# Performance work log

Hardware: AMD Instinct MI355X
Metric: run time of the kernel (lower is better)

## Reference

```python
import jax, jax.numpy as jnp
import numpy as np

T, B, E, H = 2048, 2, 1024, 16
Dh = E // H


def setup_inputs() -> dict:
    key = jax.random.key(0)
    ks = jax.random.split(key, 5)
    s = 0.02
    query = jax.random.normal(ks[0], (T, B, E), dtype=jnp.float32)
    Wq = jax.random.normal(ks[1], (E, E), dtype=jnp.float32) * s
    Wk = jax.random.normal(ks[2], (E, E), dtype=jnp.float32) * s
    Wv = jax.random.normal(ks[3], (E, E), dtype=jnp.float32) * s
    Wo = jax.random.normal(ks[4], (E, E), dtype=jnp.float32) * s
    bq = jnp.zeros((E,), jnp.float32)
    bk = jnp.zeros((E,), jnp.float32)
    bv = jnp.zeros((E,), jnp.float32)
    bo = jnp.zeros((E,), jnp.float32)
    # additive causal mask: 0 on/below diagonal, -inf above (standard fairseq usage)
    neg = jnp.finfo(jnp.float32).min
    attn_mask = jnp.where(jnp.triu(jnp.ones((T, T), jnp.bool_), k=1), neg, 0.0).astype(jnp.float32)
    return {"query": query, "Wq": Wq, "bq": bq, "Wk": Wk, "bk": bk,
            "Wv": Wv, "bv": bv, "Wo": Wo, "bo": bo, "attn_mask": attn_mask}


def reference(query, Wq, bq, Wk, bk, Wv, bv, Wo, bo, attn_mask):
    t, b, e = query.shape
    scale = Dh ** -0.5
    # self-attention projections (nn.Linear: x @ W.T + b)
    q = (query @ Wq.T + bq) * scale  # [T,B,E]
    k = query @ Wk.T + bk
    v = query @ Wv.T + bv
    # [T, B*H, Dh] -> [B*H, T, Dh]
    q = q.reshape(t, b * H, Dh).transpose(1, 0, 2)
    k = k.reshape(t, b * H, Dh).transpose(1, 0, 2)
    v = v.reshape(t, b * H, Dh).transpose(1, 0, 2)
    # explicit bmm -> softmax -> bmm (materializes [B*H, T, T])
    attn_weights = jnp.einsum('btd,bsd->bts', q, k) + attn_mask[None, :, :]
    attn_probs = jax.nn.softmax(attn_weights, axis=-1)
    attn = jnp.einsum('bts,bsd->btd', attn_probs, v)  # [B*H, T, Dh]
    attn = attn.transpose(1, 0, 2).reshape(t, b, e)  # [T,B,E]
    out = attn @ Wo.T + bo
    return out
```

## Files before the change

### kernel.cpp

```cpp
#include <hip/hip_runtime.h>


typedef __attribute__((ext_vector_type(8))) short   s16x8;
typedef __attribute__((ext_vector_type(4))) float   f32x4;
typedef __attribute__((ext_vector_type(2))) __fp16  f16x2;
typedef __attribute__((ext_vector_type(4))) __fp16  f16x4;

#define MFMA16(a, b, c) __builtin_amdgcn_mfma_f32_16x16x32_bf16((a), (b), (c), 0, 0, 0)
#define MFMApv(a, b, c) __builtin_amdgcn_mfma_f32_16x16x16f16((a), (b), (c), 0, 0, 0)

static __device__ __forceinline__ unsigned short f2bf(float f) {
    unsigned u = __float_as_uint(f);
    unsigned r = u + 0x7fffu + ((u >> 16) & 1u);
    return (unsigned short)(r >> 16);
}

static __device__ __forceinline__ void gl2lds16(const void* g, void* l) {
    __builtin_amdgcn_global_load_lds(
        (const __attribute__((address_space(1))) unsigned int*)g,
        (__attribute__((address_space(3))) unsigned int*)l, 16, 0, 0);
}

__global__ __launch_bounds__(256) void cvt_all(const float* __restrict__ query,
                                               const float* __restrict__ w0,
                                               const float* __restrict__ w1,
                                               const float* __restrict__ w2,
                                               const float* __restrict__ w3,
                                               unsigned short* __restrict__ Xb,
                                               unsigned short* __restrict__ Wcat) {
    const int bx = blockIdx.x;
    if (bx < 4096) {
        const int i = threadIdx.x;
        const float4 f = reinterpret_cast<const float4*>(query + (size_t)bx * 1024)[i];
        ushort4 u;
        u.x = f2bf(f.x); u.y = f2bf(f.y); u.z = f2bf(f.z); u.w = f2bf(f.w);
        const int mrow = (bx & 1) * 2048 + (bx >> 1);
        reinterpret_cast<ushort4*>(Xb + (size_t)mrow * 1024)[i] = u;
    } else {
        const int j   = bx - 4096;
        const int sel = j >> 10;
        const int i   = (j & 1023) * 256 + threadIdx.x;
        const float* src = (sel == 0) ? w0 : (sel == 1) ? w1 : (sel == 2) ? w2 : w3;
        const float4 f = reinterpret_cast<const float4*>(src)[i];
        ushort4 u;
        u.x = f2bf(f.x); u.y = f2bf(f.y); u.z = f2bf(f.z); u.w = f2bf(f.w);
        reinterpret_cast<ushort4*>(Wcat + (size_t)sel * 1048576)[i] = u;
    }
}

__global__ __launch_bounds__(512, 2) void gemm_qkv(const unsigned short* __restrict__ A,
                                                   const unsigned short* __restrict__ W,
                                                   const float* __restrict__ b0,
                                                   const float* __restrict__ b1,
                                                   const float* __restrict__ b2,
                                                   unsigned short* __restrict__ outQK,
                                                   __fp16* __restrict__ outV) {
    __shared__ __align__(16) unsigned short smem[65536];

    const int tid  = threadIdx.x;
    const int w    = tid >> 6;
    const int lane = tid & 63;
    const int quad = lane >> 4;
    const int c    = lane & 15;
    const int wm   = w >> 2;
    const int wn   = w & 3;

    const int id   = blockIdx.x;
    const int xcd  = id & 7;
    const int slot = id >> 3;
    const int m0 = (xcd * 2 + (slot & 1)) * 256;
    const int n0 = (slot >> 1) * 256;

    f32x4 acc[8][4];
    #pragma unroll
    for (int mi = 0; mi < 8; ++mi)
        #pragma unroll
        for (int ni = 0; ni < 4; ++ni) acc[mi][ni] = (f32x4){0.f, 0.f, 0.f, 0.f};

    const int srow = tid >> 3;
    const int g    = (tid & 7) ^ (srow & 7);
    const unsigned short* aG = A + (size_t)(m0 + srow) * 1024 + g * 8;
    const unsigned short* wG = W + (size_t)(n0 + srow) * 1024 + g * 8;
    const int loff = tid * 8;

#define STA(buf, u, k0) gl2lds16(aG + (k0) + (u) * 65536, &smem[(buf) * 32768 + (u) * 4096 + loff])
#define STB(buf, u, k0) gl2lds16(wG + (k0) + (u) * 65536, &smem[(buf) * 32768 + 16384 + (u) * 4096 + loff])

    STB(0, 0, 0); STB(0, 1, 0); STB(0, 2, 0); STB(0, 3, 0);
    STA(0, 0, 0); STA(0, 2, 0); STA(0, 1, 0); STA(0, 3, 0);
    asm volatile("s_waitcnt vmcnt(2)" ::: "memory");
    asm volatile("s_barrier" ::: "memory");

    const int cs  = c & 7;
    const int ch0 = (quad ^ cs) << 3;
    const int ch1 = ((4 + quad) ^ cs) << 3;

    s16x8 af[4][2], bl[2][2], bh[2][2];

    #pragma unroll 1
    for (int t = 0; t < 16; ++t) {
        const unsigned short* Al = &smem[(t & 1) * 32768];
        const unsigned short* Bl = Al + 16384;
        const int  nb   = (t & 1) ^ 1;
        const int  kn   = (t + 1) * 64;
        const bool more = (t < 15);

        #pragma unroll
        for (int mi = 0; mi < 4; ++mi) {
            const int row = (wm * 128 + mi * 16 + c) * 64;
            af[mi][0] = *reinterpret_cast<const s16x8*>(&Al[row + ch0]);
            af[mi][1] = *reinterpret_cast<const s16x8*>(&Al[row + ch1]);
        }
        #pragma unroll
        for (int ni = 0; ni < 2; ++ni) {
            const int row = (wn * 64 + ni * 16 + c) * 64;
            bl[ni][0] = *reinterpret_cast<const s16x8*>(&Bl[row + ch0]);
            bl[ni][1] = *reinterpret_cast<const s16x8*>(&Bl[row + ch1]);
        }
        if (more) { STB(nb, 0, kn); STB(nb, 1, kn); }
        asm volatile("s_barrier" ::: "memory");
        __builtin_amdgcn_s_setprio(1);
        #pragma unroll
        for (int mi = 0; mi < 4; ++mi)
            #pragma unroll
            for (int ni = 0; ni < 2; ++ni) {
                acc[mi][ni] = MFMA16(af[mi][0], bl[ni][0], acc[mi][ni]);
                acc[mi][ni] = MFMA16(af[mi][1], bl[ni][1], acc[mi][ni]);
            }
        __builtin_amdgcn_s_setprio(0);
        asm volatile("s_barrier" ::: "memory");

        #pragma unroll
        for (int ni = 0; ni < 2; ++ni) {
            const int row = (wn * 64 + (2 + ni) * 16 + c) * 64;
            bh[ni][0] = *reinterpret_cast<const s16x8*>(&Bl[row + ch0]);
            bh[ni][1] = *reinterpret_cast<const s16x8*>(&Bl[row + ch1]);
        }
        if (more) { STB(nb, 2, kn); STB(nb, 3, kn); }
        asm volatile("s_barrier" ::: "memory");
        __builtin_amdgcn_s_setprio(1);
        #pragma unroll
        for (int mi = 0; mi < 4; ++mi)
            #pragma unroll
            for (int ni = 0; ni < 2; ++ni) {
                acc[mi][2 + ni] = MFMA16(af[mi][0], bh[ni][0], acc[mi][2 + ni]);
                acc[mi][2 + ni] = MFMA16(af[mi][1], bh[ni][1], acc[mi][2 + ni]);
            }
        __builtin_amdgcn_s_setprio(0);
        if (more) asm volatile("s_waitcnt vmcnt(4)" ::: "memory");
        else      asm volatile("s_waitcnt vmcnt(0)" ::: "memory");
        asm volatile("s_barrier" ::: "memory");

        #pragma unroll
        for (int mi = 0; mi < 4; ++mi) {
            const int row = (wm * 128 + (4 + mi) * 16 + c) * 64;
            af[mi][0] = *reinterpret_cast<const s16x8*>(&Al[row + ch0]);
            af[mi][1] = *reinterpret_cast<const s16x8*>(&Al[row + ch1]);
        }
        if (more) { STA(nb, 0, kn); STA(nb, 2, kn); }
        asm volatile("s_barrier" ::: "memory");
        __builtin_amdgcn_s_setprio(1);
        #pragma unroll
        for (int mi = 0; mi < 4; ++mi)
            #pragma unroll
            for (int ni = 0; ni < 2; ++ni) {
                acc[4 + mi][ni] = MFMA16(af[mi][0], bl[ni][0], acc[4 + mi][ni]);
                acc[4 + mi][ni] = MFMA16(af[mi][1], bl[ni][1], acc[4 + mi][ni]);
            }
        __builtin_amdgcn_s_setprio(0);
        asm volatile("s_barrier" ::: "memory");

        if (more) { STA(nb, 1, kn); STA(nb, 3, kn); }
        asm volatile("s_barrier" ::: "memory");
        __builtin_amdgcn_s_setprio(1);
        #pragma unroll
        for (int mi = 0; mi < 4; ++mi)
            #pragma unroll
            for (int ni = 0; ni < 2; ++ni) {
                acc[4 + mi][2 + ni] = MFMA16(af[mi][0], bh[ni][0], acc[4 + mi][2 + ni]);
                acc[4 + mi][2 + ni] = MFMA16(af[mi][1], bh[ni][1], acc[4 + mi][2 + ni]);
            }
        __builtin_amdgcn_s_setprio(0);
        if (more) asm volatile("s_waitcnt vmcnt(2)" ::: "memory");
        asm volatile("s_barrier" ::: "memory");
    }
#undef STA
#undef STB

    if (n0 < 2048) {
        const float scale = (n0 < 1024) ? 0.18033688011112042f : 1.0f;
        const float* bias = (n0 < 1024) ? b0 : b1;
        #pragma unroll
        for (int ni = 0; ni < 4; ++ni) {
            const int n = n0 + wn * 64 + ni * 16 + c;
            const float bval = bias[n & 1023];
            #pragma unroll
            for (int mi = 0; mi < 8; ++mi)
                #pragma unroll
                for (int r = 0; r < 4; ++r) {
                    const int m = m0 + wm * 128 + mi * 16 + quad * 4 + r;
                    outQK[(size_t)m * 2048 + n] = f2bf((acc[mi][ni][r] + bval) * scale);
                }
        }
    } else {
        __fp16* lds16 = reinterpret_cast<__fp16*>(smem);
        #pragma unroll 1
        for (int tn = 0; tn < 2; ++tn) {
            __syncthreads();
            if ((wn >> 1) == tn) {
                #pragma unroll
                for (int ni = 0; ni < 4; ++ni) {
                    const int nLoc = (wn & 1) * 64 + ni * 16 + c;
                    const float bval = b2[(n0 - 2048) + tn * 128 + nLoc];
                    #pragma unroll
                    for (int mi = 0; mi < 8; ++mi) {
                        const int mLoc = mi * 16 + quad * 4;
                        const f16x2 lo = __builtin_amdgcn_cvt_pkrtz(acc[mi][ni][0] + bval,
                                                                    acc[mi][ni][1] + bval);
                        const f16x2 hi = __builtin_amdgcn_cvt_pkrtz(acc[mi][ni][2] + bval,
                                                                    acc[mi][ni][3] + bval);
                        uint2 st;
                        st.x = __builtin_bit_cast(unsigned int, lo);
                        st.y = __builtin_bit_cast(unsigned int, hi);
                        const int phys = wm * 16384 + nLoc * 128 +
                                         (((mLoc >> 3) ^ (nLoc & 15)) << 3) + (mLoc & 7);
                        *reinterpret_cast<uint2*>(&lds16[phys]) = st;
                    }
                }
            }
            __syncthreads();
            const int np   = tid >> 1;
            const int rg   = np >> 7;
            const int nLoc = np & 127;
            const int vcol = (n0 - 2048) + tn * 128 + nLoc;
            const int bb = m0 >> 11;
            const int tbase = (m0 & 2047) + rg * 128;
            __fp16* vdst = outV + ((size_t)((bb * 16 + (vcol >> 6)) * 64 + (vcol & 63))) * 2048 + tbase;
            #pragma unroll
            for (int j = 0; j < 8; ++j) {
                const int lc = (tid & 1) * 8 + j;
                *reinterpret_cast<uint4*>(vdst + lc * 8) =
                    *reinterpret_cast<const uint4*>(
                        &lds16[rg * 16384 + nLoc * 128 + ((lc ^ (nLoc & 15)) << 3)]);
            }
        }
    }
}

__global__ __launch_bounds__(256) void gemm_out(const unsigned short* __restrict__ A,
                                                const unsigned short* __restrict__ W,
                                                const float* __restrict__ bias,
                                                float* __restrict__ outF) {
    __shared__ __align__(16) unsigned short Al[2][64 * 64];
    __shared__ __align__(16) unsigned short Bl[2][128 * 64];

    const int tid  = threadIdx.x;
    const int w    = tid >> 6;
    const int lane = tid & 63;
    const int quad = lane >> 4;
    const int c    = lane & 15;

    const int id   = blockIdx.x;
    const int xcd  = id & 7;
    const int slot = id >> 3;
    const int m0 = (xcd * 8 + (slot & 7)) * 64;
    const int n0 = (slot >> 3) * 128;

    f32x4 acc[8];
    #pragma unroll
    for (int ni = 0; ni < 8; ++ni) acc[ni] = (f32x4){0.f, 0.f, 0.f, 0.f};

    const int srow = tid >> 3;
    const int g    = (tid & 7) ^ (srow & 7);
    const unsigned short* aG = A + (size_t)(m0 + srow) * 1024 + g * 8;
    const unsigned short* wG = W + (size_t)(n0 + srow) * 1024 + g * 8;
    const int loff = tid * 8;

    const int cs = (c & 7);

    gl2lds16(aG,             &Al[0][loff]);
    gl2lds16(aG + 32 * 1024, &Al[0][loff + 2048]);
    #pragma unroll
    for (int i = 0; i < 4; ++i)
        gl2lds16(wG + i * 32 * 1024, &Bl[0][loff + i * 2048]);

    #pragma unroll 1
    for (int kk = 0; kk < 16; ++kk) {
        __syncthreads();
        if (kk < 15) {
            const int k0n = (kk + 1) * 64;
            const int nb  = (kk + 1) & 1;
            gl2lds16(aG + k0n,             &Al[nb][loff]);
            gl2lds16(aG + k0n + 32 * 1024, &Al[nb][loff + 2048]);
            #pragma unroll
            for (int i = 0; i < 4; ++i)
                gl2lds16(wG + k0n + i * 32 * 1024, &Bl[nb][loff + i * 2048]);
        }
        const int cb = kk & 1;
        const int arow = (w * 16 + c) * 64;
        const s16x8 af0 = *reinterpret_cast<const s16x8*>(&Al[cb][arow + ((quad ^ cs) << 3)]);
        const s16x8 af1 = *reinterpret_cast<const s16x8*>(&Al[cb][arow + (((4 + quad) ^ cs) << 3)]);
        __builtin_amdgcn_s_setprio(1);
        #pragma unroll
        for (int ni = 0; ni < 8; ++ni) {
            const int brow = (ni * 16 + c) * 64;
            const s16x8 bf0 = *reinterpret_cast<const s16x8*>(&Bl[cb][brow + ((quad ^ cs) << 3)]);
            const s16x8 bf1 = *reinterpret_cast<const s16x8*>(&Bl[cb][brow + (((4 + quad) ^ cs) << 3)]);
            acc[ni] = MFMA16(af0, bf0, acc[ni]);
            acc[ni] = MFMA16(af1, bf1, acc[ni]);
        }
        __builtin_amdgcn_s_setprio(0);
    }

    #pragma unroll
    for (int ni = 0; ni < 8; ++ni) {
        const int n = n0 + ni * 16 + c;
        const float bval = bias[n];
        const int m = m0 + w * 16 + quad * 4;
        const int bb = m >> 11, t = m & 2047;
        #pragma unroll
        for (int r = 0; r < 4; ++r)
            outF[(size_t)(2 * (t + r) + bb) * 1024 + n] = acc[ni][r] + bval;
    }
}

__global__ __launch_bounds__(256, 4) void attn_kernel(const unsigned short* __restrict__ QKb,
                                                      const __fp16* __restrict__ Vt,
                                                      unsigned short* __restrict__ Ob) {
    __shared__ unsigned short Kl[2][2][64][32];
    __shared__ __fp16 Vl[2][64][64];

    const int tid  = threadIdx.x;
    const int w    = tid >> 6;
    const int lane = tid & 63;
    const int quad = lane >> 4;
    const int c    = lane & 15;

    const int id = blockIdx.x;
    const int bh = (id & 7) * 4 + ((id >> 3) & 3);
    const int kidx = id >> 5;
    const int rr   = kidx >> 3, jj = kidx & 7;
    const int a    = (rr & 1) ? (24 - 8 * rr + jj) : (31 - 8 * rr - jj);
    const int bB = bh >> 4, h = bh & 15;
    const int t0 = a * 64;
    const int trg = t0 + w * 16;
    const int nIt = a + 1;

    const unsigned short* qp = QKb + (size_t)(bB * 2048 + trg + c) * 2048 + h * 64 + quad * 8;
    const s16x8 aq0 = *reinterpret_cast<const s16x8*>(qp);
    const s16x8 aq1 = *reinterpret_cast<const s16x8*>(qp + 32);

    const int lr4 = lane >> 2, sl4 = lane & 3;
    const unsigned short* kSrc = QKb + (size_t)(bB * 2048 + w * 16 + lr4) * 2048
                                 + 1024 + h * 64 + (sl4 ^ ((lane >> 3) & 3)) * 8;
    const int vr8 = lane >> 3, sl8 = lane & 7;
    const __fp16* vSrcA = Vt + (size_t)(bh * 64 + w * 16 + vr8) * 2048 + (sl8 ^ vr8) * 8;
    const __fp16* vSrcB = vSrcA + (size_t)8 * 2048;

    f32x4 acc[4];
    float l = 0.f;
    #pragma unroll
    for (int dt = 0; dt < 4; ++dt) acc[dt] = (f32x4){0.f, 0.f, 0.f, 0.f};

    const int kswz = (quad ^ ((c >> 1) & 3)) * 8;

    {
        gl2lds16(kSrc,      &Kl[0][0][w * 16 + lr4][sl4 * 8]);
        gl2lds16(kSrc + 32, &Kl[0][1][w * 16 + lr4][sl4 * 8]);
        gl2lds16(vSrcA,     &Vl[0][w * 16 + vr8][sl8 * 8]);
        gl2lds16(vSrcB,     &Vl[0][w * 16 + 8 + vr8][sl8 * 8]);
    }

    for (int it = 0; it < nIt; ++it) {
        const int buf = it & 1;
        __syncthreads();
        if (it + 1 < nIt) {
            const size_t s1 = (size_t)(it + 1) * 64;
            const int nb = buf ^ 1;
            gl2lds16(kSrc + s1 * 2048,      &Kl[nb][0][w * 16 + lr4][sl4 * 8]);
            gl2lds16(kSrc + s1 * 2048 + 32, &Kl[nb][1][w * 16 + lr4][sl4 * 8]);
            gl2lds16(vSrcA + s1,            &Vl[nb][w * 16 + vr8][sl8 * 8]);
            gl2lds16(vSrcB + s1,            &Vl[nb][w * 16 + 8 + vr8][sl8 * 8]);
        }

        s16x8 kf[4][2];
        #pragma unroll
        for (int ns = 0; ns < 4; ++ns) {
            kf[ns][0] = *reinterpret_cast<const s16x8*>(&Kl[buf][0][ns * 16 + c][kswz]);
            kf[ns][1] = *reinterpret_cast<const s16x8*>(&Kl[buf][1][ns * 16 + c][kswz]);
        }
        f16x4 vf[4][4];
        #pragma unroll
        for (int dt = 0; dt < 4; ++dt)
            #pragma unroll
            for (int ch = 0; ch < 4; ++ch) {
                const int phys = ((2 * ch + (quad >> 1)) ^ (c & 7)) * 8 + (quad & 1) * 4;
                vf[dt][ch] = *reinterpret_cast<const f16x4*>(&Vl[buf][dt * 16 + c][phys]);
            }

        const int s0 = it * 64;
        const bool diag = (it == a);
        f32x4 sT[4];
        __builtin_amdgcn_s_setprio(1);
        #pragma unroll
        for (int ns = 0; ns < 4; ++ns) {
            f32x4 z = (f32x4){0.f, 0.f, 0.f, 0.f};
            z = MFMA16(kf[ns][0], aq0, z);
            sT[ns] = MFMA16(kf[ns][1], aq1, z);
        }
        __builtin_amdgcn_s_setprio(0);
        f16x4 pf[4];
        float lp = 0.f;
        #pragma unroll
        for (int ns = 0; ns < 4; ++ns) {
            float pv[4];
            #pragma unroll
            for (int r = 0; r < 4; ++r) pv[r] = __builtin_amdgcn_exp2f(sT[ns][r]);
            if (diag) {
                const int sb = s0 + ns * 16 + quad * 4;
                const int qg = trg + c;
                #pragma unroll
                for (int r = 0; r < 4; ++r) if (sb + r > qg) pv[r] = 0.f;
            }
            lp += (pv[0] + pv[1]) + (pv[2] + pv[3]);
            const f16x2 lo = __builtin_amdgcn_cvt_pkrtz(pv[0], pv[1]);
            const f16x2 hi = __builtin_amdgcn_cvt_pkrtz(pv[2], pv[3]);
            pf[ns] = __builtin_shufflevector(lo, hi, 0, 1, 2, 3);
        }
        l += lp;
        __builtin_amdgcn_s_setprio(1);
        #pragma unroll
        for (int dt = 0; dt < 4; ++dt)
            #pragma unroll
            for (int ns = 0; ns < 4; ++ns)
                acc[dt] = MFMApv(vf[dt][ns], pf[ns], acc[dt]);
        __builtin_amdgcn_s_setprio(0);
    }

    float lv = l;
    lv += __shfl_xor(lv, 16);
    lv += __shfl_xor(lv, 32);
    const float inv = 1.0f / lv;
    const size_t base = (size_t)(bB * 2048 + trg + c) * 1024 + h * 64;
    #pragma unroll
    for (int dt = 0; dt < 4; ++dt) {
        const unsigned u0 = (unsigned)f2bf(acc[dt][0] * inv)
                          | ((unsigned)f2bf(acc[dt][1] * inv) << 16);
        const unsigned u1 = (unsigned)f2bf(acc[dt][2] * inv)
                          | ((unsigned)f2bf(acc[dt][3] * inv) << 16);
        uint2 st; st.x = u0; st.y = u1;
        *reinterpret_cast<uint2*>(Ob + base + dt * 16 + quad * 4) = st;
    }
}

extern "C" void kernel_launch(void* const* d_in, const int* in_sizes, int n_in,
                              void* d_out, int out_size, void* d_ws, size_t ws_size,
                              hipStream_t stream) {
    const float* query = (const float*)d_in[0];
    const float* Wq    = (const float*)d_in[1];
    const float* bq    = (const float*)d_in[2];
    const float* Wk    = (const float*)d_in[3];
    const float* bk    = (const float*)d_in[4];
    const float* Wv    = (const float*)d_in[5];
    const float* bv    = (const float*)d_in[6];
    const float* Wo    = (const float*)d_in[7];
    const float* bo    = (const float*)d_in[8];

    float* out = (float*)d_out;

    unsigned short* ws    = (unsigned short*)d_ws;
    unsigned short* Xbf   = ws;
    unsigned short* Wcat  = Xbf  + (size_t)4096 * 1024;
    unsigned short* QKb   = Wcat + (size_t)4 * 1024 * 1024;
    __fp16*         Vtw   = (__fp16*)(QKb + (size_t)4096 * 2048);
    unsigned short* attnb = (unsigned short*)(Vtw + (size_t)32 * 64 * 2048);

    cvt_all<<<8192, 256, 0, stream>>>(query, Wq, Wk, Wv, Wo, Xbf, Wcat);

    gemm_qkv<<<192, 512, 0, stream>>>(Xbf, Wcat, bq, bk, bv, QKb, Vtw);

    attn_kernel<<<1024, 256, 0, stream>>>(QKb, Vtw, attnb);

    gemm_out<<<512, 256, 0, stream>>>(attnb, Wcat + (size_t)3 * 1024 * 1024,
                                      bo, out);
}
```

Before: 195.6 us.

## Restructure QKV GEMM main loop with full-tile prefetch and fewer barriers

New measurement: 193.5 us. No clear change (-1.1%).

```diff
diff --git a/kernel.cpp b/kernel.cpp
--- a/kernel.cpp
+++ b/kernel.cpp
@@ -95,94 +95,80 @@
     const int ch0 = (quad ^ cs) << 3;
     const int ch1 = ((4 + quad) ^ cs) << 3;
 
-    s16x8 af[4][2], bl[2][2], bh[2][2];
+    s16x8 af[4][2], bf[4][2];
+
+    #pragma unroll
+    for (int mi = 0; mi < 4; ++mi) {
+        const int row = (wm * 128 + mi * 16 + c) * 64;
+        af[mi][0] = *reinterpret_cast<const s16x8*>(&smem[row + ch0]);
+        af[mi][1] = *reinterpret_cast<const s16x8*>(&smem[row + ch1]);
+    }
+    #pragma unroll
+    for (int ni = 0; ni < 4; ++ni) {
+        const int row = (wn * 64 + ni * 16 + c) * 64;
+        bf[ni][0] = *reinterpret_cast<const s16x8*>(&smem[16384 + row + ch0]);
+        bf[ni][1] = *reinterpret_cast<const s16x8*>(&smem[16384 + row + ch1]);
+    }
 
     #pragma unroll 1
     for (int t = 0; t < 16; ++t) {
         const unsigned short* Al = &smem[(t & 1) * 32768];
-        const unsigned short* Bl = Al + 16384;
         const int  nb   = (t & 1) ^ 1;
         const int  kn   = (t + 1) * 64;
         const bool more = (t < 15);
 
+        if (more) {
+            STB(nb, 0, kn); STB(nb, 1, kn); STB(nb, 2, kn); STB(nb, 3, kn);
+            STA(nb, 0, kn); STA(nb, 2, kn); STA(nb, 1, kn); STA(nb, 3, kn);
+        }
+
+        __builtin_amdgcn_s_setprio(1);
+        #pragma unroll
+        for (int mi = 0; mi < 4; ++mi)
+            #pragma unroll
+            for (int ni = 0; ni < 4; ++ni) {
+                acc[mi][ni] = MFMA16(af[mi][0], bf[ni][0], acc[mi][ni]);
+                acc[mi][ni] = MFMA16(af[mi][1], bf[ni][1], acc[mi][ni]);
+            }
+        __builtin_amdgcn_s_setprio(0);
+
+        if (more) asm volatile("s_waitcnt vmcnt(8)" ::: "memory");
+        else      asm volatile("s_waitcnt vmcnt(0)" ::: "memory");
+        asm volatile("s_barrier" ::: "memory");
+
         #pragma unroll
         for (int mi = 0; mi < 4; ++mi) {
-            const int row = (wm * 128 + mi * 16 + c) * 64;
+            const int row = (wm * 128 + 64 + mi * 16 + c) * 64;
             af[mi][0] = *reinterpret_cast<const s16x8*>(&Al[row + ch0]);
             af[mi][1] = *reinterpret_cast<const s16x8*>(&Al[row + ch1]);
         }
-        #pragma unroll
-        for (int ni = 0; ni < 2; ++ni) {
-            const int row = (wn * 64 + ni * 16 + c) * 64;
-            bl[ni][0] = *reinterpret_cast<const s16x8*>(&Bl[row + ch0]);
-            bl[ni][1] = *reinterpret_cast<const s16x8*>(&Bl[row + ch1]);
-        }
-        if (more) { STB(nb, 0, kn); STB(nb, 1, kn); }
-        asm volatile("s_barrier" ::: "memory");
         __builtin_amdgcn_s_setprio(1);
         #pragma unroll
         for (int mi = 0; mi < 4; ++mi)
             #pragma unroll
-            for (int ni = 0; ni < 2; ++ni) {
-                acc[mi][ni] = MFMA16(af[mi][0], bl[ni][0], acc[mi][ni]);
-                acc[mi][ni] = MFMA16(af[mi][1], bl[ni][1], acc[mi][ni]);
+            for (int ni = 0; ni < 4; ++ni) {
+                acc[4 + mi][ni] = MFMA16(af[mi][0], bf[ni][0], acc[4 + mi][ni]);
+                acc[4 + mi][ni] = MFMA16(af[mi][1], bf[ni][1], acc[4 + mi][ni]);
             }
         __builtin_amdgcn_s_setprio(0);
-        asm volatile("s_barrier" ::: "memory");
-
-        #pragma unroll
-        for (int ni = 0; ni < 2; ++ni) {
-            const int row = (wn * 64 + (2 + ni) * 16 + c) * 64;
-            bh[ni][0] = *reinterpret_cast<const s16x8*>(&Bl[row + ch0]);
-            bh[ni][1] = *reinterpret_cast<const s16x8*>(&Bl[row + ch1]);
-        }
-        if (more) { STB(nb, 2, kn); STB(nb, 3, kn); }
-        asm volatile("s_barrier" ::: "memory");
-        __builtin_amdgcn_s_setprio(1);
-        #pragma unroll
-        for (int mi = 0; mi < 4; ++mi)
-            #pragma unroll
-            for (int ni = 0; ni < 2; ++ni) {
-                acc[mi][2 + ni] = MFMA16(af[mi][0], bh[ni][0], acc[mi][2 + ni]);
-                acc[mi][2 + ni] = MFMA16(af[mi][1], bh[ni][1], acc[mi][2 + ni]);
-            }
-        __builtin_amdgcn_s_setprio(0);
-        if (more) asm volatile("s_waitcnt vmcnt(4)" ::: "memory");
-        else      asm volatile("s_waitcnt vmcnt(0)" ::: "memory");
-        asm volatile("s_barrier" ::: "memory");
-
-        #pragma unroll
-        for (int mi = 0; mi < 4; ++mi) {
-            const int row = (wm * 128 + (4 + mi) * 16 + c) * 64;
-            af[mi][0] = *reinterpret_cast<const s16x8*>(&Al[row + ch0]);
-            af[mi][1] = *reinterpret_cast<const s16x8*>(&Al[row + ch1]);
-        }
-        if (more) { STA(nb, 0, kn); STA(nb, 2, kn); }
-        asm volatile("s_barrier" ::: "memory");
-        __builtin_amdgcn_s_setprio(1);
-        #pragma unroll
-        for (int mi = 0; mi < 4; ++mi)
-            #pragma unroll
-            for (int ni = 0; ni < 2; ++ni) {
-                acc[4 + mi][ni] = MFMA16(af[mi][0], bl[ni][0], acc[4 + mi][ni]);
-                acc[4 + mi][ni] = MFMA16(af[mi][1], bl[ni][1], acc[4 + mi][ni]);
-            }
-        __builtin_amdgcn_s_setprio(0);
-        asm volatile("s_barrier" ::: "memory");
-
-        if (more) { STA(nb, 1, kn); STA(nb, 3, kn); }
-        asm volatile("s_barrier" ::: "memory");
-        __builtin_amdgcn_s_setprio(1);
-        #pragma unroll
-        for (int mi = 0; mi < 4; ++mi)
-            #pragma unroll
-            for (int ni = 0; ni < 2; ++ni) {
-                acc[4 + mi][2 + ni] = MFMA16(af[mi][0], bh[ni][0], acc[4 + mi][2 + ni]);
-                acc[4 + mi][2 + ni] = MFMA16(af[mi][1], bh[ni][1], acc[4 + mi][2 + ni]);
-            }
-        __builtin_amdgcn_s_setprio(0);
-        if (more) asm volatile("s_waitcnt vmcnt(2)" ::: "memory");
-        asm volatile("s_barrier" ::: "memory");
+
+        if (more) {
+            asm volatile("s_waitcnt vmcnt(2)" ::: "memory");
+            asm volatile("s_barrier" ::: "memory");
+            const unsigned short* An = &smem[nb * 32768];
+            #pragma unroll
+            for (int mi = 0; mi < 4; ++mi) {
+                const int row = (wm * 128 + mi * 16 + c) * 64;
+                af[mi][0] = *reinterpret_cast<const s16x8*>(&An[row + ch0]);
+                af[mi][1] = *reinterpret_cast<const s16x8*>(&An[row + ch1]);
+            }
+            #pragma unroll
+            for (int ni = 0; ni < 4; ++ni) {
+                const int row = (wn * 64 + ni * 16 + c) * 64;
+                bf[ni][0] = *reinterpret_cast<const s16x8*>(&An[16384 + row + ch0]);
+                bf[ni][1] = *reinterpret_cast<const s16x8*>(&An[16384 + row + ch1]);
+            }
+        }
     }
 #undef STA
 #undef STB
```
